# Optimization experiments

Measured on AMD Instinct MI355X. Metric: run time of the kernel, lower is better.

## Reference

```python
import jax, jax.numpy as jnp
import numpy as np

LAYERS = 10
STACKS = 3
R = 64      # residual channels
D = 64      # dilation channels
S = 256     # skip channels
C = 256     # classes
B = 4
T = 32768


def setup_inputs() -> dict:
    key = jax.random.key(0)
    ks = jax.random.split(key, 11)
    L = LAYERS * STACKS
    def w(k, shape, fan_in):
        return jax.random.normal(k, shape, dtype=jnp.float32) / np.sqrt(fan_in)
    return {
        "y": jax.random.normal(ks[0], (B, 1, T), dtype=jnp.float32),
        "causal_w": w(ks[1], (R, 1), 1),
        "causal_b": jnp.zeros((R,), jnp.float32),
        "filt_w": w(ks[2], (L, D, R, 2), 2 * R),
        "gate_w": w(ks[3], (L, D, R, 2), 2 * R),
        "res_w": w(ks[4], (L, R, D), D),
        "skip_w": w(ks[5], (L, S, D), D),
        "end1_w": w(ks[6], (S, S), S),
        "end1_b": jnp.zeros((S,), jnp.float32),
        "end2_w": w(ks[7], (C, S), S),
        "end2_b": jnp.zeros((C,), jnp.float32),
    }


def _dil_causal_conv(x, w, d):
    # x: [B, R, T]; w: [D, R, 2] (tap 0 = t-d, tap 1 = t). Torch pads (p, p)
    # with p=d*(k-1) and the forward slices output[:, :, :T], which equals a
    # left-padded causal dilated conv: y[t] = w0 @ x[t-d] + w1 @ x[t].
    xs = jnp.pad(x, ((0, 0), (0, 0), (d, 0)))[:, :, : x.shape[-1]]
    return jnp.einsum("dr,brt->bdt", w[:, :, 0], xs) + jnp.einsum(
        "dr,brt->bdt", w[:, :, 1], x
    )


def reference(y, causal_w, causal_b, filt_w, gate_w, res_w, skip_w,
              end1_w, end1_b, end2_w, end2_b):
    # causal 1x1 conv: 1 -> R channels
    x = jnp.einsum("ri,bit->brt", causal_w, y) + causal_b[None, :, None]
    skip = jnp.zeros((y.shape[0], S, y.shape[-1]), x.dtype)
    for i in range(LAYERS * STACKS):
        d = 2 ** (i % LAYERS)
        f = jnp.tanh(_dil_causal_conv(x, filt_w[i], d))
        g = jax.nn.sigmoid(_dil_causal_conv(x, gate_w[i], d))
        out = f * g  # [B, D, T]
        skip = skip + jnp.einsum("sd,bdt->bst", skip_w[i], out)
        x = x + jnp.einsum("rd,bdt->brt", res_w[i], out)
    h = jax.nn.relu(skip)
    h = jnp.einsum("os,bst->bot", end1_w, h) + end1_b[None, :, None]
    h = jax.nn.relu(h)
    h = jnp.einsum("cs,bst->bct", end2_w, h) + end2_b[None, :, None]
    return jnp.transpose(h, (0, 2, 1))  # [B, T, C]
```

## Files before the change

### kernel.cpp

```cpp
#include <hip/hip_runtime.h>

#define TLEN 32768
#define NB 4
#define NLAYER 30

typedef short bf16x8 __attribute__((ext_vector_type(8)));
typedef float f32x16 __attribute__((ext_vector_type(16)));
#define MFMA32(a, b, c) __builtin_amdgcn_mfma_f32_32x32x16_bf16(a, b, c, 0, 0, 0)

__device__ __forceinline__ unsigned short bfh(float x) {
  unsigned int u = __float_as_uint(x);
  return (unsigned short)((u + 0x7fffu + ((u >> 16) & 1u)) >> 16);
}
__device__ __forceinline__ void fsplit(float x, unsigned short& h, unsigned short& l) {
  unsigned int u = __float_as_uint(x);
  unsigned int hb = (u + 0x7fffu + ((u >> 16) & 1u)) & 0xffff0000u;
  h = (unsigned short)(hb >> 16);
  l = bfh(x - __uint_as_float(hb));
}
__device__ __forceinline__ float bflo(unsigned int p) { return __uint_as_float(p << 16); }
__device__ __forceinline__ float bfhi2(unsigned int p) { return __uint_as_float(p & 0xffff0000u); }

__device__ __forceinline__ void split4(float4 v, uint2& h, uint2& l) {
  unsigned short h0, l0, h1, l1, h2, l2, h3, l3;
  fsplit(v.x, h0, l0); fsplit(v.y, h1, l1);
  fsplit(v.z, h2, l2); fsplit(v.w, h3, l3);
  h.x = (unsigned int)h0 | ((unsigned int)h1 << 16);
  h.y = (unsigned int)h2 | ((unsigned int)h3 << 16);
  l.x = (unsigned int)l0 | ((unsigned int)l1 << 16);
  l.y = (unsigned int)l2 | ((unsigned int)l3 << 16);
}
__device__ __forceinline__ bf16x8 asb(uint4 v) {
  union { uint4 u; bf16x8 b; } x; x.u = v; return x.b;
}
__device__ __forceinline__ bf16x8 asb2(uint2 a, uint2 b) {
  union { uint4 u; bf16x8 v; } x;
  x.u.x = a.x; x.u.y = a.y; x.u.z = b.x; x.u.w = b.y; return x.v;
}
__device__ __forceinline__ float fast_sigmoid(float x) { return 1.0f / (1.0f + __expf(-x)); }
__device__ __forceinline__ float fast_tanh(float x) { return 1.0f - 2.0f / (1.0f + __expf(2.0f * x)); }

__device__ __forceinline__ unsigned int fragOff(int s, int k, int nkc) {
  return ((((unsigned)(s >> 5) * nkc + (k >> 4)) * 2 + ((k >> 3) & 1)) * 32 + (s & 31)) * 8 + (k & 7);
}


__global__ __launch_bounds__(256) void wn_causal_k(
    const float* __restrict__ y, const float* __restrict__ cw,
    const float* __restrict__ cb, unsigned short* __restrict__ xt, int base, int cext) {
  int ti = blockIdx.x * 64 + (threadIdx.x >> 2);
  int cg = (threadIdx.x & 3) << 4;
  int b = blockIdx.y;
  float yv = y[(size_t)b * TLEN + base + ti];
  unsigned short* o = xt + ((size_t)b * cext + ti) * 128 + cg;
  uint2 h[4], l[4];
#pragma unroll
  for (int j = 0; j < 4; ++j) {
    float4 w = *(const float4*)(cw + cg + 4 * j);
    float4 bb = *(const float4*)(cb + cg + 4 * j);
    float4 v; v.x = w.x * yv + bb.x; v.y = w.y * yv + bb.y;
    v.z = w.z * yv + bb.z; v.w = w.w * yv + bb.w;
    split4(v, h[j], l[j]);
  }
  uint4 H0, H1, L0, L1;
  H0.x = h[0].x; H0.y = h[0].y; H0.z = h[1].x; H0.w = h[1].y;
  H1.x = h[2].x; H1.y = h[2].y; H1.z = h[3].x; H1.w = h[3].y;
  L0.x = l[0].x; L0.y = l[0].y; L0.z = l[1].x; L0.w = l[1].y;
  L1.x = l[2].x; L1.y = l[2].y; L1.z = l[3].x; L1.w = l[3].y;
  *(uint4*)(o) = H0; *(uint4*)(o + 8) = H1;
  *(uint4*)(o + 64) = L0; *(uint4*)(o + 72) = L1;
}

__global__ __launch_bounds__(256) void wn_prep_fg_k(
    const float* __restrict__ filt, const float* __restrict__ gate,
    unsigned short* __restrict__ fH, unsigned short* __restrict__ fL,
    unsigned short* __restrict__ gH, unsigned short* __restrict__ gL) {
  int id = blockIdx.x * 256 + threadIdx.x;
  int i = id >> 13; int rem = id & 8191; int d = rem >> 7; int k = rem & 127;
  int tap = k >> 6, r = k & 63;
  size_t sb = (size_t)i * 8192;
  unsigned int off = fragOff(d, k, 8);
  unsigned short h, l;
  fsplit(filt[sb + d * 128 + r * 2 + tap], h, l); fH[sb + off] = h; fL[sb + off] = l;
  fsplit(gate[sb + d * 128 + r * 2 + tap], h, l); gH[sb + off] = h; gL[sb + off] = l;
}

__global__ __launch_bounds__(256) void wn_repackA_k(
    const float* __restrict__ src, unsigned short* __restrict__ dH,
    unsigned short* __restrict__ dL, int kShift, int mkShift) {
  int id = blockIdx.x * 256 + threadIdx.x;
  int layer = id >> mkShift;
  int rem = id & ((1 << mkShift) - 1);
  int s = rem >> kShift;
  int k = rem & ((1 << kShift) - 1);
  int nkc = 1 << (kShift - 4);
  unsigned int off = fragOff(s, k, nkc);
  size_t base = (size_t)layer << mkShift;
  unsigned short h, l;
  fsplit(src[base + rem], h, l);
  dH[base + off] = h; dL[base + off] = l;
}

__global__ __launch_bounds__(256, 3) void wn_layer_k(
    const unsigned short* __restrict__ xin, unsigned short* __restrict__ xout,
    unsigned short* __restrict__ outp,
    const unsigned short* __restrict__ fH, const unsigned short* __restrict__ fL,
    const unsigned short* __restrict__ gH, const unsigned short* __restrict__ gL,
    const unsigned short* __restrict__ rH, const unsigned short* __restrict__ rL,
    int dil, int ti_start, int lo, int cext, int tc) {
  __shared__ unsigned short Xs[64 * 260];
  __shared__ unsigned short Os[64 * 132];

  const int tid = threadIdx.x;
  const int lane = tid & 63, wave = tid >> 6;
  const int q = lane >> 5, ln = lane & 31;
  const int b = blockIdx.y;
  const int ti0 = ti_start + (int)blockIdx.x * 64;
  const unsigned short* xb = xin + (size_t)b * cext * 128;

  {
    int row = tid >> 2, cg = (tid & 3) << 4;
    const unsigned short* src = xb + (size_t)(ti0 + row) * 128 + cg;
    unsigned short* dh = &Xs[row * 260 + 64 + cg];
    unsigned short* dl = &Xs[row * 260 + 192 + cg];
    {
      uint4 h0 = *(const uint4*)(src);
      uint4 h1 = *(const uint4*)(src + 8);
      uint4 l0 = *(const uint4*)(src + 64);
      uint4 l1 = *(const uint4*)(src + 72);
      uint2 t;
      t.x = h0.x; t.y = h0.y; *(uint2*)(dh + 0) = t;
      t.x = h0.z; t.y = h0.w; *(uint2*)(dh + 4) = t;
      t.x = h1.x; t.y = h1.y; *(uint2*)(dh + 8) = t;
      t.x = h1.z; t.y = h1.w; *(uint2*)(dh + 12) = t;
      t.x = l0.x; t.y = l0.y; *(uint2*)(dl + 0) = t;
      t.x = l0.z; t.y = l0.w; *(uint2*)(dl + 4) = t;
      t.x = l1.x; t.y = l1.y; *(uint2*)(dl + 8) = t;
      t.x = l1.z; t.y = l1.w; *(uint2*)(dl + 12) = t;
    }
    int ts = ti0 + row - dil;
    dh = &Xs[row * 260 + cg];
    dl = &Xs[row * 260 + 128 + cg];
    if (ts >= 0) {
      const unsigned short* s2 = xb + (size_t)ts * 128 + cg;
      uint4 h0 = *(const uint4*)(s2);
      uint4 h1 = *(const uint4*)(s2 + 8);
      uint4 l0 = *(const uint4*)(s2 + 64);
      uint4 l1 = *(const uint4*)(s2 + 72);
      uint2 t;
      t.x = h0.x; t.y = h0.y; *(uint2*)(dh + 0) = t;
      t.x = h0.z; t.y = h0.w; *(uint2*)(dh + 4) = t;
      t.x = h1.x; t.y = h1.y; *(uint2*)(dh + 8) = t;
      t.x = h1.z; t.y = h1.w; *(uint2*)(dh + 12) = t;
      t.x = l0.x; t.y = l0.y; *(uint2*)(dl + 0) = t;
      t.x = l0.z; t.y = l0.w; *(uint2*)(dl + 4) = t;
      t.x = l1.x; t.y = l1.y; *(uint2*)(dl + 8) = t;
      t.x = l1.z; t.y = l1.w; *(uint2*)(dl + 12) = t;
    } else {
      uint2 z; z.x = 0; z.y = 0;
#pragma unroll
      for (int j = 0; j < 4; ++j) { *(uint2*)(dh + 4 * j) = z; *(uint2*)(dl + 4 * j) = z; }
    }
  }

  const int dblk = wave >> 1, tblk = wave & 1;

  uint4 afh[8], agh[8];
  const uint4* pfh = (const uint4*)fH;
  const uint4* pfl = (const uint4*)fL;
  const uint4* pgh = (const uint4*)gH;
  const uint4* pgl = (const uint4*)gL;
  const int abase = dblk * 512 + q * 32 + ln;
#pragma unroll
  for (int kc = 0; kc < 8; ++kc) {
    afh[kc] = pfh[abase + kc * 64];
    agh[kc] = pgh[abase + kc * 64];
  }
  __syncthreads();

  f32x16 accF, accG;
#pragma unroll
  for (int i = 0; i < 16; ++i) { accF[i] = 0.f; accG[i] = 0.f; }

  const unsigned short* xrow = &Xs[(tblk * 32 + ln) * 260];
#pragma unroll
  for (int kc = 0; kc < 8; ++kc) {
    uint4 fl = pfl[abase + kc * 64];
    uint4 gl = pgl[abase + kc * 64];
    uint2 h0 = *(const uint2*)(xrow + kc * 16 + q * 8);
    uint2 h1 = *(const uint2*)(xrow + kc * 16 + q * 8 + 4);
    uint2 l0 = *(const uint2*)(xrow + 128 + kc * 16 + q * 8);
    uint2 l1 = *(const uint2*)(xrow + 128 + kc * 16 + q * 8 + 4);
    bf16x8 bh = asb2(h0, h1), bl = asb2(l0, l1);
    accF = MFMA32(asb(afh[kc]), bh, accF);
    accF = MFMA32(asb(afh[kc]), bl, accF);
    accF = MFMA32(asb(fl), bh, accF);
    accG = MFMA32(asb(agh[kc]), bh, accG);
    accG = MFMA32(asb(agh[kc]), bl, accG);
    accG = MFMA32(asb(gl), bh, accG);
  }

  {
    int trow = tblk * 32 + ln;
    unsigned short* orow = &Os[trow * 132 + dblk * 32];
#pragma unroll
    for (int g = 0; g < 4; ++g) {
      int dofs = 8 * g + 4 * q;
      unsigned short oh[4], ol[4];
#pragma unroll
      for (int j = 0; j < 4; ++j) {
        float f = fast_tanh(accF[g * 4 + j]) * fast_sigmoid(accG[g * 4 + j]);
        fsplit(f, oh[j], ol[j]);
      }
      uint2 hv, lv;
      hv.x = (unsigned int)oh[0] | ((unsigned int)oh[1] << 16);
      hv.y = (unsigned int)oh[2] | ((unsigned int)oh[3] << 16);
      lv.x = (unsigned int)ol[0] | ((unsigned int)ol[1] << 16);
      lv.y = (unsigned int)ol[2] | ((unsigned int)ol[3] << 16);
      *(uint2*)(orow + dofs) = hv;
      *(uint2*)(orow + 64 + dofs) = lv;
    }
  }
  __syncthreads();

  if (ti0 >= lo) {
    int row = tid >> 2, c16 = (tid & 3) << 4;
    const unsigned short* sp = &Os[row * 132 + c16];
    uint2 a0 = *(const uint2*)(sp);
    uint2 a1 = *(const uint2*)(sp + 4);
    uint2 a2 = *(const uint2*)(sp + 8);
    uint2 a3 = *(const uint2*)(sp + 12);
    uint4 v0, v1;
    v0.x = a0.x; v0.y = a0.y; v0.z = a1.x; v0.w = a1.y;
    v1.x = a2.x; v1.y = a2.y; v1.z = a3.x; v1.w = a3.y;
    unsigned short* dp = outp + ((size_t)b * tc + (ti0 - lo + row)) * 64 + c16;
    *(uint4*)(dp) = v0;
    *(uint4*)(dp + 8) = v1;
  }

  {
    const int rblk = wave >> 1, tb2 = wave & 1;
    const int rb4 = rblk * 256 + q * 32 + ln;
    const uint4* prh = (const uint4*)rH;
    const uint4* prl = (const uint4*)rL;
    uint4 arh[4], arl[4];
#pragma unroll
    for (int kc = 0; kc < 4; ++kc) {
      arh[kc] = prh[rb4 + kc * 64];
      arl[kc] = prl[rb4 + kc * 64];
    }
    f32x16 accR;
#pragma unroll
    for (int i = 0; i < 16; ++i) accR[i] = 0.f;
    const int t = tb2 * 32 + ln;
    const unsigned short* orow = &Os[t * 132];
#pragma unroll
    for (int kc = 0; kc < 4; ++kc) {
      uint2 h0 = *(const uint2*)(orow + kc * 16 + q * 8);
      uint2 h1 = *(const uint2*)(orow + kc * 16 + q * 8 + 4);
      uint2 l0 = *(const uint2*)(orow + 64 + kc * 16 + q * 8);
      uint2 l1 = *(const uint2*)(orow + 64 + kc * 16 + q * 8 + 4);
      bf16x8 bh = asb2(h0, h1), bl = asb2(l0, l1);
      accR = MFMA32(asb(arh[kc]), bh, accR);
      accR = MFMA32(asb(arh[kc]), bl, accR);
      accR = MFMA32(asb(arl[kc]), bh, accR);
    }
    __syncthreads();
#pragma unroll
    for (int g = 0; g < 4; ++g) {
      int rbase = rblk * 32 + 8 * g + 4 * q;
      uint2 xh = *(const uint2*)&Xs[t * 260 + 64 + rbase];
      uint2 xl = *(const uint2*)&Xs[t * 260 + 192 + rbase];
      float4 v;
      v.x = accR[g * 4 + 0] + bflo(xh.x) + bflo(xl.x);
      v.y = accR[g * 4 + 1] + bfhi2(xh.x) + bfhi2(xl.x);
      v.z = accR[g * 4 + 2] + bflo(xh.y) + bflo(xl.y);
      v.w = accR[g * 4 + 3] + bfhi2(xh.y) + bfhi2(xl.y);
      uint2 hv, lv;
      split4(v, hv, lv);
      *(uint2*)&Os[t * 132 + rbase] = hv;
      *(uint2*)&Os[t * 132 + 64 + rbase] = lv;
    }
    __syncthreads();
    int row = tid >> 2, seg = (tid & 3) << 5;
    const unsigned short* sp = &Os[row * 132 + seg];
    uint2 a0 = *(const uint2*)(sp);
    uint2 a1 = *(const uint2*)(sp + 4);
    uint2 a2 = *(const uint2*)(sp + 8);
    uint2 a3 = *(const uint2*)(sp + 12);
    uint2 a4 = *(const uint2*)(sp + 16);
    uint2 a5 = *(const uint2*)(sp + 20);
    uint2 a6 = *(const uint2*)(sp + 24);
    uint2 a7 = *(const uint2*)(sp + 28);
    uint4 w0, w1, w2, w3;
    w0.x = a0.x; w0.y = a0.y; w0.z = a1.x; w0.w = a1.y;
    w1.x = a2.x; w1.y = a2.y; w1.z = a3.x; w1.w = a3.y;
    w2.x = a4.x; w2.y = a4.y; w2.z = a5.x; w2.w = a5.y;
    w3.x = a6.x; w3.y = a6.y; w3.z = a7.x; w3.w = a7.y;
    unsigned short* dp = xout + ((size_t)b * cext + ti0 + row) * 128 + seg;
    *(uint4*)(dp) = w0; *(uint4*)(dp + 8) = w1;
    *(uint4*)(dp + 16) = w2; *(uint4*)(dp + 24) = w3;
  }
}

__global__ __launch_bounds__(256, 3) void wn_skipend_k(
    const unsigned short* __restrict__ outs,
    const unsigned short* __restrict__ sH, const unsigned short* __restrict__ sL,
    const unsigned short* __restrict__ e1H, const unsigned short* __restrict__ e1L,
    const float* __restrict__ b1,
    const unsigned short* __restrict__ e2H, const unsigned short* __restrict__ e2L,
    const float* __restrict__ b2, float* __restrict__ out, int c0, int tc) {
  __shared__ unsigned short SM[64 * 260];

  const int tid = threadIdx.x;
  const int lane = tid & 63, wave = tid >> 6;
  const int q = lane >> 5, ln = lane & 31;
  const int b = blockIdx.y;
  const int tl0 = (int)blockIdx.x * 64;

  f32x16 acc[4];
#pragma unroll
  for (int a = 0; a < 4; ++a)
#pragma unroll
    for (int i = 0; i < 16; ++i) acc[a][i] = 0.f;

  const int r0 = tid >> 3, c80 = (tid & 7) << 3;
  const int r1 = r0 + 32;

  const unsigned short* ob = outs + ((size_t)b * tc + tl0) * 64;
  const size_t lstride = (size_t)NB * tc * 64;

  uint4 ld0, ld1;
  ld0 = *(const uint4*)(ob + r0 * 64 + c80);
  ld1 = *(const uint4*)(ob + r1 * 64 + c80);
  int cur = 0;
  {
    unsigned short* base = SM;
    uint2 t0; t0.x = ld0.x; t0.y = ld0.y;
    uint2 t1; t1.x = ld0.z; t1.y = ld0.w;
    *(uint2*)&base[r0 * 68 + c80] = t0;
    *(uint2*)&base[r0 * 68 + c80 + 4] = t1;
    uint2 t2; t2.x = ld1.x; t2.y = ld1.y;
    uint2 t3; t3.x = ld1.z; t3.y = ld1.w;
    *(uint2*)&base[r1 * 68 + c80] = t2;
    *(uint2*)&base[r1 * 68 + c80 + 4] = t3;
  }

  const int ab = wave * 512 + q * 32 + ln;
  for (int i = 0; i < NLAYER; ++i) {
    if (i + 1 < NLAYER) {
      const unsigned short* src = ob + (size_t)(i + 1) * lstride;
      ld0 = *(const uint4*)(src + r0 * 64 + c80);
      ld1 = *(const uint4*)(src + r1 * 64 + c80);
    }
    __syncthreads();
    const unsigned short* sbuf = SM + cur * (64 * 68);
    const uint4* pa = (const uint4*)sH + (size_t)i * 2048;
    const uint4* pl = (const uint4*)sL + (size_t)i * 2048;
#pragma unroll
    for (int kc = 0; kc < 4; ++kc) {
#pragma unroll
      for (int sblk = 0; sblk < 2; ++sblk) {
        uint4 ah = pa[ab + sblk * 256 + kc * 64];
        uint4 al = pl[ab + sblk * 256 + kc * 64];
#pragma unroll
        for (int tt = 0; tt < 2; ++tt) {
          uint2 b0 = *(const uint2*)&sbuf[(tt * 32 + ln) * 68 + kc * 16 + q * 8];
          uint2 b1v = *(const uint2*)&sbuf[(tt * 32 + ln) * 68 + kc * 16 + q * 8 + 4];
          bf16x8 bb = asb2(b0, b1v);
          acc[sblk * 2 + tt] = MFMA32(asb(ah), bb, acc[sblk * 2 + tt]);
          acc[sblk * 2 + tt] = MFMA32(asb(al), bb, acc[sblk * 2 + tt]);
        }
      }
    }
    if (i + 1 < NLAYER) {
      unsigned short* base = SM + (cur ^ 1) * (64 * 68);
      uint2 t0; t0.x = ld0.x; t0.y = ld0.y;
      uint2 t1; t1.x = ld0.z; t1.y = ld0.w;
      *(uint2*)&base[r0 * 68 + c80] = t0;
      *(uint2*)&base[r0 * 68 + c80 + 4] = t1;
      uint2 t2; t2.x = ld1.x; t2.y = ld1.y;
      uint2 t3; t3.x = ld1.z; t3.y = ld1.w;
      *(uint2*)&base[r1 * 68 + c80] = t2;
      *(uint2*)&base[r1 * 68 + c80 + 4] = t3;
    }
    cur ^= 1;
  }
  __syncthreads();

#pragma unroll
  for (int sblk = 0; sblk < 2; ++sblk)
#pragma unroll
    for (int tt = 0; tt < 2; ++tt) {
      int t = tt * 32 + ln;
#pragma unroll
      for (int g = 0; g < 4; ++g) {
        int s = wave * 64 + sblk * 32 + 8 * g + 4 * q;
        unsigned short h0 = bfh(fmaxf(acc[sblk * 2 + tt][g * 4 + 0], 0.f));
        unsigned short h1 = bfh(fmaxf(acc[sblk * 2 + tt][g * 4 + 1], 0.f));
        unsigned short h2 = bfh(fmaxf(acc[sblk * 2 + tt][g * 4 + 2], 0.f));
        unsigned short h3 = bfh(fmaxf(acc[sblk * 2 + tt][g * 4 + 3], 0.f));
        uint2 hv;
        hv.x = (unsigned int)h0 | ((unsigned int)h1 << 16);
        hv.y = (unsigned int)h2 | ((unsigned int)h3 << 16);
        *(uint2*)&SM[t * 260 + s] = hv;
      }
    }
  __syncthreads();

#pragma unroll
  for (int a = 0; a < 4; ++a)
#pragma unroll
    for (int i = 0; i < 16; ++i) acc[a][i] = 0.f;
  const uint4* p1h = (const uint4*)e1H;
  const uint4* p1l = (const uint4*)e1L;
  const int eb = wave * 2048 + q * 32 + ln;
#pragma unroll 4
  for (int kc = 0; kc < 16; ++kc) {
#pragma unroll
    for (int ot = 0; ot < 2; ++ot) {
      uint4 ah = p1h[eb + ot * 1024 + kc * 64];
      uint4 al = p1l[eb + ot * 1024 + kc * 64];
#pragma unroll
      for (int tt = 0; tt < 2; ++tt) {
        uint2 b0 = *(const uint2*)&SM[(tt * 32 + ln) * 260 + kc * 16 + q * 8];
        uint2 b1v = *(const uint2*)&SM[(tt * 32 + ln) * 260 + kc * 16 + q * 8 + 4];
        bf16x8 bb = asb2(b0, b1v);
        acc[ot * 2 + tt] = MFMA32(asb(ah), bb, acc[ot * 2 + tt]);
        acc[ot * 2 + tt] = MFMA32(asb(al), bb, acc[ot * 2 + tt]);
      }
    }
  }
  __syncthreads();
#pragma unroll
  for (int ot = 0; ot < 2; ++ot)
#pragma unroll
    for (int tt = 0; tt < 2; ++tt) {
      int t = tt * 32 + ln;
#pragma unroll
      for (int g = 0; g < 4; ++g) {
        int o = wave * 64 + ot * 32 + 8 * g + 4 * q;
        float4 bb = *(const float4*)(b1 + o);
        unsigned short h0 = bfh(fmaxf(acc[ot * 2 + tt][g * 4 + 0] + bb.x, 0.f));
        unsigned short h1 = bfh(fmaxf(acc[ot * 2 + tt][g * 4 + 1] + bb.y, 0.f));
        unsigned short h2 = bfh(fmaxf(acc[ot * 2 + tt][g * 4 + 2] + bb.z, 0.f));
        unsigned short h3 = bfh(fmaxf(acc[ot * 2 + tt][g * 4 + 3] + bb.w, 0.f));
        uint2 hv;
        hv.x = (unsigned int)h0 | ((unsigned int)h1 << 16);
        hv.y = (unsigned int)h2 | ((unsigned int)h3 << 16);
        *(uint2*)&SM[t * 260 + o] = hv;
      }
    }
  __syncthreads();

#pragma unroll
  for (int a = 0; a < 4; ++a)
#pragma unroll
    for (int i = 0; i < 16; ++i) acc[a][i] = 0.f;
  const uint4* p2h = (const uint4*)e2H;
  const uint4* p2l = (const uint4*)e2L;
#pragma unroll 4
  for (int kc = 0; kc < 16; ++kc) {
#pragma unroll
    for (int ot = 0; ot < 2; ++ot) {
      uint4 ah = p2h[eb + ot * 1024 + kc * 64];
      uint4 al = p2l[eb + ot * 1024 + kc * 64];
#pragma unroll
      for (int tt = 0; tt < 2; ++tt) {
        uint2 b0 = *(const uint2*)&SM[(tt * 32 + ln) * 260 + kc * 16 + q * 8];
        uint2 b1v = *(const uint2*)&SM[(tt * 32 + ln) * 260 + kc * 16 + q * 8 + 4];
        bf16x8 bb = asb2(b0, b1v);
        acc[ot * 2 + tt] = MFMA32(asb(ah), bb, acc[ot * 2 + tt]);
        acc[ot * 2 + tt] = MFMA32(asb(al), bb, acc[ot * 2 + tt]);
      }
    }
  }
  __syncthreads();

  float* SMf = (float*)SM;
#pragma unroll
  for (int hp = 0; hp < 2; ++hp) {
#pragma unroll
    for (int ot = 0; ot < 2; ++ot)
#pragma unroll
      for (int g = 0; g < 4; ++g) {
        int o = wave * 64 + ot * 32 + 8 * g + 4 * q;
        float4 bb = *(const float4*)(b2 + o);
        float2 v0, v1;
        v0.x = acc[ot * 2 + hp][g * 4 + 0] + bb.x;
        v0.y = acc[ot * 2 + hp][g * 4 + 1] + bb.y;
        v1.x = acc[ot * 2 + hp][g * 4 + 2] + bb.z;
        v1.y = acc[ot * 2 + hp][g * 4 + 3] + bb.w;
        *(float2*)&SMf[ln * 260 + o] = v0;
        *(float2*)&SMf[ln * 260 + o + 2] = v1;
      }
    __syncthreads();
    {
      int row = tid >> 3, c32 = (tid & 7) << 5;
      float* op = out + ((size_t)b * TLEN + c0 + tl0 + hp * 32 + row) * 256 + c32;
      const float* spf = &SMf[row * 260 + c32];
#pragma unroll
      for (int j = 0; j < 8; ++j) *(float4*)(op + 4 * j) = *(const float4*)(spf + 4 * j);
    }
    if (hp == 0) __syncthreads();
  }
}

extern "C" void kernel_launch(void* const* d_in, const int* in_sizes, int n_in,
                              void* d_out, int out_size, void* d_ws,
                              size_t ws_size, hipStream_t stream) {
  (void)in_sizes; (void)n_in; (void)out_size;
  const float* y     = (const float*)d_in[0];
  const float* cw    = (const float*)d_in[1];
  const float* cb    = (const float*)d_in[2];
  const float* filt  = (const float*)d_in[3];
  const float* gate  = (const float*)d_in[4];
  const float* resw  = (const float*)d_in[5];
  const float* skipw = (const float*)d_in[6];
  const float* w1    = (const float*)d_in[7];
  const float* b1    = (const float*)d_in[8];
  const float* w2    = (const float*)d_in[9];
  const float* b2    = (const float*)d_in[10];
  float* out = (float*)d_out;

  int P[NLAYER];
  P[NLAYER - 1] = 0;
  for (int i = NLAYER - 1; i >= 1; --i) {
    int d = 1 << (i % 10);
    P[i - 1] = ((P[i] + d + 63) / 64) * 64;
  }
  const int LO = ((P[0] + 1 + 63) / 64) * 64;

  const size_t nFG = (size_t)NLAYER * 8192;
  const size_t nRes = (size_t)NLAYER * 4096;
  const size_t nSkip = (size_t)NLAYER * 16384;
  const size_t nE = 65536;
  const size_t wTot = 4 * nFG + 2 * nRes + 2 * nSkip + 4 * nE;

  auto need = [&](int tcv, int lov) -> size_t {
    return 2ull * NB * (size_t)(tcv + lov) * 256
         + (size_t)NLAYER * NB * (size_t)tcv * 64 * 2
         + wTot * 2;
  };
  int tc, lo, nchunk;
  if (ws_size >= need(TLEN, 0)) {
    tc = TLEN; lo = 0; nchunk = 1;
  } else if (ws_size >= need(TLEN / 2, LO)) {
    tc = TLEN / 2; lo = LO; nchunk = 2;
  } else {
    tc = TLEN / 4; lo = LO; nchunk = 4;
  }
  const int cext = tc + lo;

  const size_t NXTr = (size_t)NB * cext * 128;
  unsigned short* xtA = (unsigned short*)d_ws;
  unsigned short* xtB = xtA + NXTr;
  unsigned short* outsB = xtB + NXTr;
  const size_t outsN = (size_t)NLAYER * NB * (size_t)tc * 64;
  unsigned short* wb = outsB + outsN;
  unsigned short* fH = wb;            unsigned short* fL = fH + nFG;
  unsigned short* gH = fL + nFG;      unsigned short* gL = gH + nFG;
  unsigned short* rH = gL + nFG;      unsigned short* rL = rH + nRes;
  unsigned short* sH = rL + nRes;     unsigned short* sL = sH + nSkip;
  unsigned short* e1H = sL + nSkip;   unsigned short* e1L = e1H + nE;
  unsigned short* e2H = e1L + nE;     unsigned short* e2L = e2H + nE;

  wn_prep_fg_k<<<dim3(NLAYER * 8192 / 256), dim3(256), 0, stream>>>(
      filt, gate, fH, fL, gH, gL);
  wn_repackA_k<<<dim3(NLAYER * 4096 / 256), dim3(256), 0, stream>>>(resw, rH, rL, 6, 12);
  wn_repackA_k<<<dim3(NLAYER * 16384 / 256), dim3(256), 0, stream>>>(skipw, sH, sL, 6, 14);
  wn_repackA_k<<<dim3(65536 / 256), dim3(256), 0, stream>>>(w1, e1H, e1L, 8, 16);
  wn_repackA_k<<<dim3(65536 / 256), dim3(256), 0, stream>>>(w2, e2H, e2L, 8, 16);

  for (int c = 0; c < nchunk; ++c) {
    int c0 = c * tc;
    int loc = (c == 0) ? 0 : lo;
    int ext = tc + loc;
    int base = c0 - loc;
    wn_causal_k<<<dim3(ext / 64, NB), dim3(256), 0, stream>>>(y, cw, cb, xtA, base, cext);
    unsigned short* xi = xtA;
    unsigned short* xo = xtB;
    for (int i = 0; i < NLAYER; ++i) {
      int d = 1 << (i % 10);
      int Pe = (c == 0) ? 0 : P[i];
      int nt = tc + Pe;
      wn_layer_k<<<dim3(nt / 64, NB), dim3(256), 0, stream>>>(
          xi, xo, outsB + (size_t)i * NB * (size_t)tc * 64,
          fH + (size_t)i * 8192, fL + (size_t)i * 8192,
          gH + (size_t)i * 8192, gL + (size_t)i * 8192,
          rH + (size_t)i * 4096, rL + (size_t)i * 4096,
          d, loc - Pe, loc, cext, tc);
      unsigned short* tmp = xi; xi = xo; xo = tmp;
    }
    wn_skipend_k<<<dim3(tc / 64, NB), dim3(256), 0, stream>>>(
        outsB, sH, sL, e1H, e1L, b1, e2H, e2L, b2, out, c0, tc);
  }
}
```

Measured before the change: 2.200 ms.

## Store gated activations in MFMA-fragment tile layout and load skip operands directly

The layer kernel now writes each 64-timestep tile of gated outputs in a layout that matches the MFMA B-operand fragments. The skip/end kernel can then read B fragments straight from global memory with one uint4 per lane. This removes the LDS double-buffer staging and the per-layer __syncthreads from the 30-layer skip accumulation loop. The trade-off is that global loads now sit directly in front of the MFMAs with no explicit prefetch, so the code relies on the hardware and compiler to hide that latency.

```diff
diff --git a/kernel.cpp b/kernel.cpp
--- a/kernel.cpp
+++ b/kernel.cpp
@@ -224,18 +224,19 @@
   __syncthreads();
 
   if (ti0 >= lo) {
-    int row = tid >> 2, c16 = (tid & 3) << 4;
-    const unsigned short* sp = &Os[row * 132 + c16];
-    uint2 a0 = *(const uint2*)(sp);
-    uint2 a1 = *(const uint2*)(sp + 4);
-    uint2 a2 = *(const uint2*)(sp + 8);
-    uint2 a3 = *(const uint2*)(sp + 12);
+    int tile = (ti0 - lo) >> 6;
+    int t = tid & 63, fg = tid >> 6;
+    const unsigned short* sp = &Os[t * 132];
+    uint2 a0 = *(const uint2*)(sp + fg * 8);
+    uint2 a1 = *(const uint2*)(sp + fg * 8 + 4);
+    uint2 c0 = *(const uint2*)(sp + 32 + fg * 8);
+    uint2 c1 = *(const uint2*)(sp + 32 + fg * 8 + 4);
     uint4 v0, v1;
     v0.x = a0.x; v0.y = a0.y; v0.z = a1.x; v0.w = a1.y;
-    v1.x = a2.x; v1.y = a2.y; v1.z = a3.x; v1.w = a3.y;
-    unsigned short* dp = outp + ((size_t)b * tc + (ti0 - lo + row)) * 64 + c16;
-    *(uint4*)(dp) = v0;
-    *(uint4*)(dp + 8) = v1;
+    v1.x = c0.x; v1.y = c0.y; v1.z = c1.x; v1.w = c1.y;
+    unsigned short* dpb = outp + ((size_t)b * (tc >> 6) + tile) * 4096;
+    *(uint4*)(dpb + fg * 512 + t * 8) = v0;
+    *(uint4*)(dpb + (fg + 4) * 512 + t * 8) = v1;
   }
 
   {
@@ -324,69 +325,31 @@
 #pragma unroll
     for (int i = 0; i < 16; ++i) acc[a][i] = 0.f;
 
-  const int r0 = tid >> 3, c80 = (tid & 7) << 3;
-  const int r1 = r0 + 32;
-
-  const unsigned short* ob = outs + ((size_t)b * tc + tl0) * 64;
-  const size_t lstride = (size_t)NB * tc * 64;
-
-  uint4 ld0, ld1;
-  ld0 = *(const uint4*)(ob + r0 * 64 + c80);
-  ld1 = *(const uint4*)(ob + r1 * 64 + c80);
-  int cur = 0;
-  {
-    unsigned short* base = SM;
-    uint2 t0; t0.x = ld0.x; t0.y = ld0.y;
-    uint2 t1; t1.x = ld0.z; t1.y = ld0.w;
-    *(uint2*)&base[r0 * 68 + c80] = t0;
-    *(uint2*)&base[r0 * 68 + c80 + 4] = t1;
-    uint2 t2; t2.x = ld1.x; t2.y = ld1.y;
-    uint2 t3; t3.x = ld1.z; t3.y = ld1.w;
-    *(uint2*)&base[r1 * 68 + c80] = t2;
-    *(uint2*)&base[r1 * 68 + c80 + 4] = t3;
-  }
-
+  const int ntiles = tc >> 6;
+  const size_t lstride4 = (size_t)NB * tc * 8;
+  const uint4* pbl = (const uint4*)outs + ((size_t)b * ntiles + blockIdx.x) * 512
+                   + q * 64 + ln;
   const int ab = wave * 512 + q * 32 + ln;
+
   for (int i = 0; i < NLAYER; ++i) {
-    if (i + 1 < NLAYER) {
-      const unsigned short* src = ob + (size_t)(i + 1) * lstride;
-      ld0 = *(const uint4*)(src + r0 * 64 + c80);
-      ld1 = *(const uint4*)(src + r1 * 64 + c80);
-    }
-    __syncthreads();
-    const unsigned short* sbuf = SM + cur * (64 * 68);
+    const uint4* pb = pbl + (size_t)i * lstride4;
     const uint4* pa = (const uint4*)sH + (size_t)i * 2048;
     const uint4* pl = (const uint4*)sL + (size_t)i * 2048;
 #pragma unroll
     for (int kc = 0; kc < 4; ++kc) {
+      uint4 bb0 = pb[kc * 128];
+      uint4 bb1 = pb[kc * 128 + 32];
 #pragma unroll
       for (int sblk = 0; sblk < 2; ++sblk) {
         uint4 ah = pa[ab + sblk * 256 + kc * 64];
         uint4 al = pl[ab + sblk * 256 + kc * 64];
-#pragma unroll
-        for (int tt = 0; tt < 2; ++tt) {
-          uint2 b0 = *(const uint2*)&sbuf[(tt * 32 + ln) * 68 + kc * 16 + q * 8];
-          uint2 b1v = *(const uint2*)&sbuf[(tt * 32 + ln) * 68 + kc * 16 + q * 8 + 4];
-          bf16x8 bb = asb2(b0, b1v);
-          acc[sblk * 2 + tt] = MFMA32(asb(ah), bb, acc[sblk * 2 + tt]);
-          acc[sblk * 2 + tt] = MFMA32(asb(al), bb, acc[sblk * 2 + tt]);
-        }
-      }
-    }
-    if (i + 1 < NLAYER) {
-      unsigned short* base = SM + (cur ^ 1) * (64 * 68);
-      uint2 t0; t0.x = ld0.x; t0.y = ld0.y;
-      uint2 t1; t1.x = ld0.z; t1.y = ld0.w;
-      *(uint2*)&base[r0 * 68 + c80] = t0;
-      *(uint2*)&base[r0 * 68 + c80 + 4] = t1;
-      uint2 t2; t2.x = ld1.x; t2.y = ld1.y;
-      uint2 t3; t3.x = ld1.z; t3.y = ld1.w;
-      *(uint2*)&base[r1 * 68 + c80] = t2;
-      *(uint2*)&base[r1 * 68 + c80 + 4] = t3;
-    }
-    cur ^= 1;
-  }
-  __syncthreads();
+        acc[sblk * 2 + 0] = MFMA32(asb(ah), asb(bb0), acc[sblk * 2 + 0]);
+        acc[sblk * 2 + 0] = MFMA32(asb(al), asb(bb0), acc[sblk * 2 + 0]);
+        acc[sblk * 2 + 1] = MFMA32(asb(ah), asb(bb1), acc[sblk * 2 + 1]);
+        acc[sblk * 2 + 1] = MFMA32(asb(al), asb(bb1), acc[sblk * 2 + 1]);
+      }
+    }
+  }
 
 #pragma unroll
   for (int sblk = 0; sblk < 2; ++sblk)
```

Result: faster. 2.109 ms (-4.2%).
